# Kernel optimization log

Hardware: AMD Instinct MI355X
Metric: run time of the kernel (lower is better)

The kernel has to match this reference:

```python
import jax, jax.numpy as jnp
import numpy as np

S = 192          # spatial_size
N = 100000       # active input sites
CIN, M, M2, NCLS = 3, 32, 64, 50
EPS = 1e-4       # scn BatchNorm eps
OFFS = np.array([[dx, dy, dz] for dx in (-1, 0, 1) for dy in (-1, 0, 1) for dz in (-1, 0, 1)], dtype=np.int64)


def _build_nbr(coords, size):
    # coords: [n,3] unique int64. Returns [n,27] int32 neighbor index (-1 = inactive site),
    # i.e. the submanifold-convolution rulebook built via sorted-key hashing.
    n = coords.shape[0]
    keys = (coords[:, 0] * size + coords[:, 1]) * size + coords[:, 2]
    order = np.argsort(keys)
    sk = keys[order]
    nbr = np.full((n, 27), -1, dtype=np.int32)
    for k, off in enumerate(OFFS):
        nc = coords + off
        ok = np.all((nc >= 0) & (nc < size), axis=1)
        qk = (nc[:, 0] * size + nc[:, 1]) * size + nc[:, 2]
        pos = np.searchsorted(sk, qk).clip(0, n - 1)
        hit = ok & (sk[pos] == qk)
        nbr[hit, k] = order[pos[hit]].astype(np.int32)
    return nbr


def setup_inputs() -> dict:
    rng = np.random.default_rng(0)
    raw = rng.integers(0, S, size=(130000, 3), dtype=np.int64)
    keys = (raw[:, 0] * S + raw[:, 1]) * S + raw[:, 2]
    _, first = np.unique(keys, return_index=True)
    coords = raw[np.sort(first)][:N]          # N unique active voxels
    nbr_fine = _build_nbr(coords, S)
    # stride-2 / filter-2 downsample rulebook: coarse sites = unique(coords // 2)
    S2 = S // 2
    cc = coords // 2
    ckeys = (cc[:, 0] * S2 + cc[:, 1]) * S2 + cc[:, 2]
    uk, parent = np.unique(ckeys, return_inverse=True)
    ccoords = np.column_stack((uk // (S2 * S2), (uk // S2) % S2, uk % S2))
    nbr_coarse = _build_nbr(ccoords, S2)
    offset_id = (coords[:, 0] % 2) * 4 + (coords[:, 1] % 2) * 2 + coords[:, 2] % 2
    key = jax.random.key(0)
    ks = jax.random.split(key, 8)
    def w(k, shape, fan):
        return jax.random.normal(k, shape, jnp.float32) * (1.0 / np.sqrt(fan))
    return dict(
        coords=jnp.asarray(coords, jnp.int32),
        features=jax.random.normal(ks[0], (N, CIN), jnp.float32),
        nbr_fine=jnp.asarray(nbr_fine),
        nbr_coarse=jnp.asarray(nbr_coarse),
        parent=jnp.asarray(parent.astype(np.int32)),
        offset_id=jnp.asarray(offset_id.astype(np.int32)),
        num_coarse=int(uk.shape[0]),
        w_in=w(ks[1], (27, CIN, M), 27 * CIN),
        w_b1=w(ks[2], (27, M, M), 27 * M),
        w_down=w(ks[3], (8, M, M2), 8 * M),
        w_b2=w(ks[4], (27, M2, M2), 27 * M2),
        w_up=w(ks[5], (8, M2, M), 8 * M2),
        w_b3=w(ks[6], (27, 2 * M, M), 27 * 2 * M),
        g1=jnp.ones((M,)), b1=jnp.zeros((M,)),
        gd=jnp.ones((M,)), bd=jnp.zeros((M,)),
        g2=jnp.ones((M2,)), b2=jnp.zeros((M2,)),
        gu=jnp.ones((M2,)), bu=jnp.zeros((M2,)),
        g3=jnp.ones((2 * M,)), b3=jnp.zeros((2 * M,)),
        go=jnp.ones((M,)), bo=jnp.zeros((M,)),
        w_lin=w(ks[7], (M, NCLS), M),
        b_lin=jnp.zeros((NCLS,)),
    )


def _subm_conv(f, nbr, W):
    # f: [n,Cin], nbr: [n,27] (-1 = inactive), W: [27,Cin,Cout]
    mask = nbr >= 0
    g = f[jnp.where(mask, nbr, 0)] * mask[..., None]  # [n,27,Cin]
    return jnp.einsum('nkc,kcd->nd', g, W)


def _bnrelu(f, gamma, beta):
    mu = f.mean(0)
    var = ((f - mu) ** 2).mean(0)
    return jax.nn.relu((f - mu) * (gamma / jnp.sqrt(var + EPS)) + beta)


def _down(f, parent, off_id, W, nc):
    # strided 2^3 conv: out[parent] += W[offset(child)] @ f[child]
    out = jnp.zeros((nc, W.shape[2]), f.dtype)
    for o in range(8):
        sel = (off_id == o)[:, None].astype(f.dtype)
        out = out + jax.ops.segment_sum((f * sel) @ W[o], parent, num_segments=nc)
    return out


def _up(g, parent, off_id, W):
    # 2^3 deconv back to fine sites
    gp = g[parent]
    out = jnp.zeros((gp.shape[0], W.shape[2]), g.dtype)
    for o in range(8):
        out = out + (off_id == o)[:, None].astype(g.dtype) * (gp @ W[o])
    return out


def reference(coords, features, nbr_fine, nbr_coarse, parent, offset_id, num_coarse,
              w_in, w_b1, w_down, w_b2, w_up, w_b3,
              g1, b1, gd, bd, g2, b2, gu, bu, g3, b3, go, bo, w_lin, b_lin):
    # InputLayer (coords unique -> identity) + SubmanifoldConvolution(CIN->M)
    f = _subm_conv(features, nbr_fine, w_in)
    # UNet level 0 block (pre-activation)
    f = _subm_conv(_bnrelu(f, g1, b1), nbr_fine, w_b1)
    skip = f
    # downsample: BNReLU + Convolution(M->M2, 2, 2)
    g = _down(_bnrelu(f, gd, bd), parent, offset_id, w_down, num_coarse)
    # UNet level 1 block
    g = _subm_conv(_bnrelu(g, g2, b2), nbr_coarse, w_b2)
    # upsample: BNReLU + Deconvolution(M2->M, 2, 2)
    u = _up(_bnrelu(g, gu, bu), parent, offset_id, w_up)
    # JoinTable + block (2M -> M)
    f = jnp.concatenate([skip, u], axis=1)
    f = _subm_conv(_bnrelu(f, g3, b3), nbr_fine, w_b3)
    # top-level BatchNormReLU(M) + OutputLayer + Linear head
    f = _bnrelu(f, go, bo)
    return f @ w_lin + b_lin
```

## Files before the change

### kernel.cpp

```cpp
#include <hip/hip_runtime.h>

#define EPS_BN 1e-4f
constexpr int BLK = 256;
constexpr int ECAPC = 1856;
constexpr int NCOPY = 8;

__global__ __launch_bounds__(64) void build_fine_k(
    const int* __restrict__ nbr, int n, int* __restrict__ cnt, int* __restrict__ ent) {
  int i = blockIdx.x * 64 + threadIdx.x;
  if (i >= n) return;
  int c = 0;
  const int* nr = nbr + (size_t)i * 27;
  int* er = ent + (size_t)i * 27;
#pragma unroll 1
  for (int k = 0; k < 27; ++k) {
    int j = nr[k];
    if (j >= 0) er[c++] = (k << 18) | j;
  }
  cnt[i] = c;
}

__global__ __launch_bounds__(64) void build_subm4_k(
    const int* __restrict__ nbr, int n,
    int* __restrict__ segP, int* __restrict__ ent) {
  int T = blockIdx.x, r = threadIdx.x;
  int i = T * 64 + r;
  bool valid = i < n;
  int base = 0;
#pragma unroll 1
  for (int k = 0; k < 27; ++k) {
    int j = valid ? nbr[(size_t)i * 27 + k] : -1;
    bool act = j >= 0;
    unsigned long long mb = __ballot(act);
    int cntk = __popcll(mb);
    int pre = __popcll(mb & ((1ull << r) - 1));
    if (act) ent[(size_t)T * ECAPC + base + pre] = (r << 23) | (k << 18) | j;
    int padded = (cntk + 3) & ~3;
    if (r < padded - cntk) ent[(size_t)T * ECAPC + base + cntk + r] = -1;
    base += padded;
  }
  if (r == 0) segP[T] = base;
}

__global__ __launch_bounds__(BLK) void child_scatter_k(
    const int* __restrict__ parent, const int* __restrict__ offid, int n,
    int* __restrict__ ccnt, int* __restrict__ cent) {
  int i = blockIdx.x * BLK + threadIdx.x;
  if (i >= n) return;
  int p = parent[i];
  int slot = atomicAdd(&ccnt[p], 1);
  cent[p * 8 + slot] = i | (offid[i] << 25);
}

template <int CI, int CO, int MODE>
__global__ __launch_bounds__(BLK) void tconvA_k(
    const float* __restrict__ in, const int* __restrict__ ent, const int* __restrict__ cnt,
    const int* __restrict__ parent, const int* __restrict__ offid,
    const float* __restrict__ W, float* __restrict__ out, int n,
    float* __restrict__ osums) {
  constexpr int LANES = CO / 4, SLOTS = BLK / LANES, RPS = 64 / SLOTS;
  __shared__ float red[2 * CO];
  int t = threadIdx.x;
  for (int idx = t; idx < 2 * CO; idx += BLK) red[idx] = 0.f;
  __syncthreads();
  int slot = t / LANES, lane = t % LANES, g = lane * 4;
  int T = blockIdx.x;
  float ssum[4] = {0, 0, 0, 0}, ssq[4] = {0, 0, 0, 0};
#pragma unroll 1
  for (int rr = 0; rr < RPS; ++rr) {
    int row = T * 64 + slot * RPS + rr;
    bool vrow = row < n;
    float a0 = 0.f, a1 = 0.f, a2 = 0.f, a3 = 0.f;
    int ec = 0;
    if (vrow) ec = (MODE == 2) ? 1 : cnt[row];
#pragma unroll 1
    for (int e = 0; e < ec; ++e) {
      int k, j;
      if constexpr (MODE == 0) {
        int v = ent[(size_t)row * 27 + e];
        k = (v >> 18) & 31; j = v & 0x3FFFF;
      } else if constexpr (MODE == 1) {
        int v = ent[(size_t)row * 8 + e];
        k = v >> 25; j = v & 0x1FFFFFF;
      } else {
        k = offid[row]; j = parent[row];
      }
      const float* Wk = W + (size_t)k * (CI * CO) + g;
      const float* xr = in + (size_t)j * CI;
#pragma unroll
      for (int h = 0; h < CI / 32; ++h) {
        float4 xv[8];
#pragma unroll
        for (int c4 = 0; c4 < 8; ++c4)
          xv[c4] = *reinterpret_cast<const float4*>(xr + h * 32 + c4 * 4);
#pragma unroll
        for (int c4 = 0; c4 < 8; ++c4) {
          float xs[4] = {xv[c4].x, xv[c4].y, xv[c4].z, xv[c4].w};
#pragma unroll
          for (int q = 0; q < 4; ++q) {
            float4 wv = *reinterpret_cast<const float4*>(Wk + (size_t)(h * 32 + c4 * 4 + q) * CO);
            a0 = fmaf(xs[q], wv.x, a0);
            a1 = fmaf(xs[q], wv.y, a1);
            a2 = fmaf(xs[q], wv.z, a2);
            a3 = fmaf(xs[q], wv.w, a3);
          }
        }
      }
    }
    if (vrow)
      *reinterpret_cast<float4*>(out + (size_t)row * CO + g) = make_float4(a0, a1, a2, a3);
    ssum[0] += a0; ssum[1] += a1; ssum[2] += a2; ssum[3] += a3;
    ssq[0] = fmaf(a0, a0, ssq[0]); ssq[1] = fmaf(a1, a1, ssq[1]);
    ssq[2] = fmaf(a2, a2, ssq[2]); ssq[3] = fmaf(a3, a3, ssq[3]);
  }
#pragma unroll
  for (int q = 0; q < 4; ++q) {
    atomicAdd(&red[g + q], ssum[q]);
    atomicAdd(&red[CO + g + q], ssq[q]);
  }
  __syncthreads();
  int copy = blockIdx.x & (NCOPY - 1);
  if (t < 2 * CO) atomicAdd(&osums[copy * 2 * CO + t], red[t]);
}

template <int CI, int CO>
__global__ __launch_bounds__(BLK) void tconvB_k(
    const float* __restrict__ in, const int* __restrict__ segP,
    const int* __restrict__ ent, int ecap,
    const float* __restrict__ sums, const float* __restrict__ gm,
    const float* __restrict__ bt, float invn,
    const float* __restrict__ W, float* __restrict__ out, int n,
    float* __restrict__ osums) {
  constexpr int AP = CO + 2;
  constexpr int XP = CI + 2;
  constexpr int CHUNK = 128;
  __shared__ float lacc[64 * AP];
  __shared__ float lx[CHUNK * XP];
  __shared__ int   lent[CHUNK];
  __shared__ float lst[2 * CI];
  int t = threadIdx.x, T = blockIdx.x;
  if (t < CI) {
    float s = 0.f, q = 0.f;
#pragma unroll
    for (int cp = 0; cp < NCOPY; ++cp) { s += sums[cp * 2 * CI + t]; q += sums[cp * 2 * CI + CI + t]; }
    float mu = s * invn, var = q * invn - mu * mu;
    float sc = gm[t] / sqrtf(var + EPS_BN);
    lst[t] = sc; lst[CI + t] = bt[t] - mu * sc;
  }
  for (int idx = t; idx < 64 * AP; idx += BLK) lacc[idx] = 0.f;
  int P = segP[T];
  const int* entT = ent + (size_t)T * ecap;
  int slot = t >> 4, g = (t & 15) * 4;
  __syncthreads();

#pragma unroll 1
  for (int c0 = 0; c0 < P; c0 += CHUNK) {
    int lim = min(P - c0, CHUNK);
    if (t < CHUNK) lent[t] = (t < lim) ? entT[c0 + t] : -1;
    for (int idx = t; idx < CHUNK * 16; idx += BLK) {
      int pr = idx >> 4, cq = idx & 15;
      int ev = (pr < lim) ? entT[c0 + pr] : -1;
      float4 v = make_float4(0.f, 0.f, 0.f, 0.f);
      if (ev >= 0) {
        int j = ev & 0x3FFFF;
        float4 x = *reinterpret_cast<const float4*>(in + (size_t)j * CI + cq * 4);
        int cb = cq * 4;
        float y0 = fmaf(x.x, lst[cb + 0], lst[CI + cb + 0]);
        float y1 = fmaf(x.y, lst[cb + 1], lst[CI + cb + 1]);
        float y2 = fmaf(x.z, lst[cb + 2], lst[CI + cb + 2]);
        float y3 = fmaf(x.w, lst[cb + 3], lst[CI + cb + 3]);
        v = make_float4(y0 > 0.f ? y0 : 0.f, y1 > 0.f ? y1 : 0.f,
                        y2 > 0.f ? y2 : 0.f, y3 > 0.f ? y3 : 0.f);
      }
      *reinterpret_cast<float4*>(&lx[pr * XP + cq * 4]) = v;
    }
    __syncthreads();
#pragma unroll 1
    for (int gr = slot; gr * 4 < lim; gr += 16) {
      int p0 = gr * 4;
      int e0 = lent[p0];
      int k = (e0 >> 18) & 31;
      const float* Wk = W + (size_t)k * (CI * CO) + g;
      int rr[4];
      float acc[4][4];
#pragma unroll
      for (int pp = 0; pp < 4; ++pp) {
        int ev = lent[p0 + pp];
        rr[pp] = ev >= 0 ? ((ev >> 23) & 63) : -1;
        acc[pp][0] = acc[pp][1] = acc[pp][2] = acc[pp][3] = 0.f;
      }
#pragma unroll 4
      for (int c4 = 0; c4 < CI / 4; ++c4) {
        int cb = c4 * 4;
        float xs[4][4];
#pragma unroll
        for (int pp = 0; pp < 4; ++pp) {
          float4 xv = *reinterpret_cast<const float4*>(&lx[(p0 + pp) * XP + cb]);
          xs[pp][0] = xv.x; xs[pp][1] = xv.y; xs[pp][2] = xv.z; xs[pp][3] = xv.w;
        }
#pragma unroll
        for (int q = 0; q < 4; ++q) {
          float4 w4 = *reinterpret_cast<const float4*>(Wk + (size_t)(cb + q) * CO);
#pragma unroll
          for (int pp = 0; pp < 4; ++pp) {
            acc[pp][0] = fmaf(xs[pp][q], w4.x, acc[pp][0]);
            acc[pp][1] = fmaf(xs[pp][q], w4.y, acc[pp][1]);
            acc[pp][2] = fmaf(xs[pp][q], w4.z, acc[pp][2]);
            acc[pp][3] = fmaf(xs[pp][q], w4.w, acc[pp][3]);
          }
        }
      }
#pragma unroll
      for (int pp = 0; pp < 4; ++pp) {
        if (rr[pp] >= 0) {
          float* ap = &lacc[rr[pp] * AP + g];
          atomicAdd(ap + 0, acc[pp][0]);
          atomicAdd(ap + 1, acc[pp][1]);
          atomicAdd(ap + 2, acc[pp][2]);
          atomicAdd(ap + 3, acc[pp][3]);
        }
      }
    }
    __syncthreads();
  }

  for (int idx = t; idx < 64 * (CO / 4); idx += BLK) {
    int r = idx / (CO / 4), c4 = idx - r * (CO / 4);
    int row = T * 64 + r;
    if (row < n)
      *reinterpret_cast<float4*>(out + (size_t)row * CO + c4 * 4) =
          *reinterpret_cast<const float4*>(&lacc[r * AP + c4 * 4]);
  }
  int copy = blockIdx.x & (NCOPY - 1);
  if (t < CO) {
    float s = 0.f, ss = 0.f;
#pragma unroll 4
    for (int r = 0; r < 64; ++r) {
      float x = lacc[r * AP + t];
      s += x; ss = fmaf(x, x, ss);
    }
    atomicAdd(&osums[copy * 2 * CO + t], s);
    atomicAdd(&osums[copy * 2 * CO + CO + t], ss);
  }
}

template <int C>
__global__ __launch_bounds__(BLK) void bnact_k(
    const float* __restrict__ in, const float* __restrict__ sums,
    const float* __restrict__ gm, const float* __restrict__ bt, float invn,
    float* __restrict__ outp, int n) {
  __shared__ float lst[2 * C];
  int t = threadIdx.x;
  if (t < C) {
    float s = 0.f, q = 0.f;
#pragma unroll
    for (int cp = 0; cp < NCOPY; ++cp) { s += sums[cp * 2 * C + t]; q += sums[cp * 2 * C + C + t]; }
    float mu = s * invn, var = q * invn - mu * mu;
    float sc = gm[t] / sqrtf(var + EPS_BN);
    lst[t] = sc; lst[C + t] = bt[t] - mu * sc;
  }
  __syncthreads();
  int total = n * (C / 4);
  const float4* in4 = reinterpret_cast<const float4*>(in);
  float4* out4 = reinterpret_cast<float4*>(outp);
  for (int idx = blockIdx.x * BLK + t; idx < total; idx += gridDim.x * BLK) {
    int cb = (idx & (C / 4 - 1)) * 4;
    float4 x = in4[idx];
    float v[4] = {x.x, x.y, x.z, x.w};
#pragma unroll
    for (int q = 0; q < 4; ++q) {
      float y = fmaf(v[q], lst[cb + q], lst[C + cb + q]);
      v[q] = y > 0.f ? y : 0.f;
    }
    out4[idx] = make_float4(v[0], v[1], v[2], v[3]);
  }
}

__global__ __launch_bounds__(BLK) void bncat_k(
    const float* __restrict__ fa, const float* __restrict__ sA,
    const float* __restrict__ gA, const float* __restrict__ bA,
    const float* __restrict__ fb, const float* __restrict__ sB,
    const float* __restrict__ gB, const float* __restrict__ bB,
    float invn, float* __restrict__ acat, int n) {
  __shared__ float lst[128];
  int t = threadIdx.x;
  if (t < 64) {
    int half = t >> 5, c = t & 31;
    const float* ss = half ? sB : sA;
    const float* gg = half ? gB : gA;
    const float* bb = half ? bB : bA;
    float s = 0.f, q = 0.f;
#pragma unroll
    for (int cp = 0; cp < NCOPY; ++cp) { s += ss[cp * 64 + c]; q += ss[cp * 64 + 32 + c]; }
    float mu = s * invn, var = q * invn - mu * mu;
    float sc = gg[c] / sqrtf(var + EPS_BN);
    lst[half * 64 + c] = sc; lst[half * 64 + 32 + c] = bb[c] - mu * sc;
  }
  __syncthreads();
  int total = n * 16;
  for (int idx = blockIdx.x * BLK + t; idx < total; idx += gridDim.x * BLK) {
    int row = idx >> 4, c4 = idx & 15;
    int half = c4 >> 3, cc = (c4 & 7) * 4;
    const float* src = half ? fb : fa;
    float4 x = *reinterpret_cast<const float4*>(src + (size_t)row * 32 + cc);
    const float* L = lst + half * 64;
    float v[4] = {x.x, x.y, x.z, x.w};
#pragma unroll
    for (int q = 0; q < 4; ++q) {
      float y = fmaf(v[q], L[cc + q], L[32 + cc + q]);
      v[q] = y > 0.f ? y : 0.f;
    }
    *reinterpret_cast<float4*>(acat + (size_t)row * 64 + c4 * 4) = make_float4(v[0], v[1], v[2], v[3]);
  }
}

__global__ __launch_bounds__(BLK) void conv_in_k(
    const float* __restrict__ feat, const int* __restrict__ nbr,
    const float* __restrict__ W, float* __restrict__ out, int n,
    float* __restrict__ osums) {
  int i = blockIdx.x * BLK + threadIdx.x;
  bool valid = i < n;
  float acc[32];
#pragma unroll
  for (int c = 0; c < 32; ++c) acc[c] = 0.f;
#pragma unroll 1
  for (int k = 0; k < 27; ++k) {
    int j = valid ? nbr[(size_t)i * 27 + k] : -1;
    if (j < 0) continue;
    float x0 = feat[j * 3 + 0], x1 = feat[j * 3 + 1], x2 = feat[j * 3 + 2];
    const float* w0 = W + k * 96;
#pragma unroll
    for (int co = 0; co < 8; ++co) {
      float4 a = *reinterpret_cast<const float4*>(w0 + co * 4);
      float4 b = *reinterpret_cast<const float4*>(w0 + 32 + co * 4);
      float4 cc = *reinterpret_cast<const float4*>(w0 + 64 + co * 4);
      acc[4*co+0] = fmaf(x0, a.x, fmaf(x1, b.x, fmaf(x2, cc.x, acc[4*co+0])));
      acc[4*co+1] = fmaf(x0, a.y, fmaf(x1, b.y, fmaf(x2, cc.y, acc[4*co+1])));
      acc[4*co+2] = fmaf(x0, a.z, fmaf(x1, b.z, fmaf(x2, cc.z, acc[4*co+2])));
      acc[4*co+3] = fmaf(x0, a.w, fmaf(x1, b.w, fmaf(x2, cc.w, acc[4*co+3])));
    }
  }
  if (valid) {
    float* o = out + (size_t)i * 32;
#pragma unroll
    for (int co = 0; co < 8; ++co)
      *reinterpret_cast<float4*>(o + co * 4) = make_float4(acc[4*co], acc[4*co+1], acc[4*co+2], acc[4*co+3]);
  }
  __shared__ float red[2][4][32];
  int w = threadIdx.x >> 6;
#pragma unroll
  for (int c = 0; c < 32; ++c) {
    float v = acc[c], q = acc[c] * acc[c];
#pragma unroll
    for (int off = 32; off; off >>= 1) {
      v += __shfl_down(v, off);
      q += __shfl_down(q, off);
    }
    if ((threadIdx.x & 63) == 0) { red[0][w][c] = v; red[1][w][c] = q; }
  }
  __syncthreads();
  if (threadIdx.x < 64) {
    int kind = threadIdx.x >> 5, c = threadIdx.x & 31;
    float s = red[kind][0][c] + red[kind][1][c] + red[kind][2][c] + red[kind][3][c];
    atomicAdd(&osums[(blockIdx.x & (NCOPY - 1)) * 64 + kind * 32 + c], s);
  }
}

__global__ __launch_bounds__(BLK) void head_k(
    const float* __restrict__ fin, const float* __restrict__ sums,
    const float* __restrict__ gm, const float* __restrict__ bt, float inv_n,
    const float* __restrict__ Wl, const float* __restrict__ bl,
    float* __restrict__ out, int n) {
  __shared__ float lw[32 * 50];
  __shared__ float lb[52];
  __shared__ float lst[64];
  int t = threadIdx.x;
  if (t < 32) {
    float s = 0.f, q = 0.f;
#pragma unroll
    for (int cp = 0; cp < NCOPY; ++cp) { s += sums[cp * 64 + t]; q += sums[cp * 64 + 32 + t]; }
    float mu = s * inv_n, var = q * inv_n - mu * mu;
    float sc = gm[t] / sqrtf(var + EPS_BN);
    lst[t] = sc; lst[32 + t] = bt[t] - mu * sc;
  }
  for (int idx = t; idx < 1600; idx += BLK) lw[idx] = Wl[idx];
  if (t < 50) lb[t] = bl[t];
  __syncthreads();
  int i = blockIdx.x * BLK + t;
  if (i >= n) return;
  float x[32];
  const float* fj = fin + (size_t)i * 32;
#pragma unroll
  for (int c4 = 0; c4 < 8; ++c4) {
    float4 v = *reinterpret_cast<const float4*>(fj + c4 * 4);
    float vs[4] = {v.x, v.y, v.z, v.w};
#pragma unroll
    for (int q = 0; q < 4; ++q) {
      int c = c4 * 4 + q;
      float y = fmaf(vs[q], lst[c], lst[32 + c]);
      x[c] = y > 0.f ? y : 0.f;
    }
  }
  float acc[50];
#pragma unroll
  for (int co = 0; co < 50; ++co) acc[co] = lb[co];
#pragma unroll 4
  for (int c = 0; c < 32; ++c) {
#pragma unroll
    for (int co = 0; co < 50; ++co) acc[co] = fmaf(x[c], lw[c * 50 + co], acc[co]);
  }
  float* o = out + (size_t)i * 50;
#pragma unroll
  for (int co = 0; co < 25; ++co)
    *reinterpret_cast<float2*>(o + co * 2) = make_float2(acc[co * 2], acc[co * 2 + 1]);
}

extern "C" void kernel_launch(void* const* d_in, const int* in_sizes, int n_in,
                              void* d_out, int out_size, void* d_ws, size_t ws_size,
                              hipStream_t stream) {
  const float* feat   = (const float*)d_in[1];
  const int*   nbrF   = (const int*)d_in[2];
  const int*   nbrC   = (const int*)d_in[3];
  const int*   parent = (const int*)d_in[4];
  const int*   offid  = (const int*)d_in[5];
  const float* w_in   = (const float*)d_in[7];
  const float* w_b1   = (const float*)d_in[8];
  const float* w_down = (const float*)d_in[9];
  const float* w_b2   = (const float*)d_in[10];
  const float* w_up   = (const float*)d_in[11];
  const float* w_b3   = (const float*)d_in[12];
  const float* g1v = (const float*)d_in[13], *b1v = (const float*)d_in[14];
  const float* gdv = (const float*)d_in[15], *bdv = (const float*)d_in[16];
  const float* g2v = (const float*)d_in[17], *b2v = (const float*)d_in[18];
  const float* guv = (const float*)d_in[19], *buv = (const float*)d_in[20];
  const float* g3v = (const float*)d_in[21], *b3v = (const float*)d_in[22];
  const float* gov = (const float*)d_in[23], *bov = (const float*)d_in[24];
  const float* w_lin = (const float*)d_in[25];
  const float* b_lin = (const float*)d_in[26];
  float* out = (float*)d_out;

  int N  = in_sizes[4];
  int NC = in_sizes[3] / 27;
  int ntF = (N + 63) / 64, ntC = (NC + 63) / 64;

  size_t szF = (size_t)N * 32;
  size_t szG = (size_t)NC * 64;
  size_t SB  = (size_t)N * 64;

  float* ws = (float*)d_ws;
  float* S1 = ws;
  float* S2 = S1 + SB;
  float* S3 = S2 + SB;
  float* S4 = S3 + szF;
  float* S5 = S4 + szF;
  float* sums1 = S5 + szG;
  float* sumsD = sums1 + 8 * 64;
  float* sums2 = sumsD + 8 * 64;
  float* sumsU = sums2 + 8 * 128;
  float* sums4 = sumsU + 8 * 128;
  float* sums5 = sums4 + 8 * 64;
  int* ccnt = (int*)(sums5 + 8 * 64);
  int* cent = ccnt + NC;
  int* cntF = cent + (size_t)NC * 8;
  int* entF = cntF + N;
  int* segPC = entF + (size_t)N * 27;
  int* entC  = segPC + ntC;

  hipMemsetAsync(sums1, 0, (4096 + NC) * sizeof(float), stream);

  int gridN = (N + BLK - 1) / BLK;
  int agrid = 1024;
  float invN = 1.f / (float)N, invC = 1.f / (float)NC;

  build_fine_k<<<ntF, 64, 0, stream>>>(nbrF, N, cntF, entF);
  build_subm4_k<<<ntC, 64, 0, stream>>>(nbrC, NC, segPC, entC);
  child_scatter_k<<<gridN, BLK, 0, stream>>>(parent, offid, N, ccnt, cent);

  conv_in_k<<<gridN, BLK, 0, stream>>>(feat, nbrF, w_in, S1, N, sums1);
  bnact_k<32><<<agrid, BLK, 0, stream>>>(S1, sums1, g1v, b1v, invN, S2, N);

  tconvA_k<32, 32, 0><<<ntF, BLK, 0, stream>>>(
      S2, entF, cntF, nullptr, nullptr, w_b1, S3, N, sumsD);
  bnact_k<32><<<agrid, BLK, 0, stream>>>(S3, sumsD, gdv, bdv, invN, S4, N);

  tconvA_k<32, 64, 1><<<ntC, BLK, 0, stream>>>(
      S4, cent, ccnt, nullptr, nullptr, w_down, S5, NC, sums2);

  tconvB_k<64, 64><<<ntC, BLK, 0, stream>>>(
      S5, segPC, entC, ECAPC, sums2, g2v, b2v, invC, w_b2, S1, NC, sumsU);
  bnact_k<64><<<agrid, BLK, 0, stream>>>(S1, sumsU, guv, buv, invC, S5, NC);

  tconvA_k<64, 32, 2><<<ntF, BLK, 0, stream>>>(
      S5, nullptr, nullptr, parent, offid, w_up, S4, N, sums4);

  bncat_k<<<agrid, BLK, 0, stream>>>(
      S3, sumsD, g3v, b3v, S4, sums4, g3v + 32, b3v + 32, invN, S2, N);

  tconvA_k<64, 32, 0><<<ntF, BLK, 0, stream>>>(
      S2, entF, cntF, nullptr, nullptr, w_b3, S3, N, sums5);

  head_k<<<gridN, BLK, 0, stream>>>(S3, sums5, gov, bov, invN, w_lin, b_lin, out, N);
}
```

Before: 552.8 us.

## Restructure coarse subm conv: per-offset segments, LDS-staged weights, 128-row tiles

Measured after the change: 581.0 us. +5.1%, slower.

```diff
diff --git a/kernel.cpp b/kernel.cpp
--- a/kernel.cpp
+++ b/kernel.cpp
@@ -2,7 +2,7 @@
 
 #define EPS_BN 1e-4f
 constexpr int BLK = 256;
-constexpr int ECAPC = 1856;
+constexpr int ECAPC = 1728;
 constexpr int NCOPY = 8;
 
 __global__ __launch_bounds__(64) void build_fine_k(
@@ -20,26 +20,24 @@
   cnt[i] = c;
 }
 
-__global__ __launch_bounds__(64) void build_subm4_k(
+__global__ __launch_bounds__(64) void build_subm_k(
     const int* __restrict__ nbr, int n,
-    int* __restrict__ segP, int* __restrict__ ent) {
+    int* __restrict__ seg, int* __restrict__ ent) {
   int T = blockIdx.x, r = threadIdx.x;
   int i = T * 64 + r;
   bool valid = i < n;
   int base = 0;
+  if (r == 0) seg[T * 28] = 0;
 #pragma unroll 1
   for (int k = 0; k < 27; ++k) {
     int j = valid ? nbr[(size_t)i * 27 + k] : -1;
     bool act = j >= 0;
     unsigned long long mb = __ballot(act);
-    int cntk = __popcll(mb);
     int pre = __popcll(mb & ((1ull << r) - 1));
-    if (act) ent[(size_t)T * ECAPC + base + pre] = (r << 23) | (k << 18) | j;
-    int padded = (cntk + 3) & ~3;
-    if (r < padded - cntk) ent[(size_t)T * ECAPC + base + cntk + r] = -1;
-    base += padded;
-  }
-  if (r == 0) segP[T] = base;
+    if (act) ent[(size_t)T * ECAPC + base + pre] = (r << 22) | j;
+    base += __popcll(mb);
+    if (r == 0) seg[T * 28 + k + 1] = base;
+  }
 }
 
 __global__ __launch_bounds__(BLK) void child_scatter_k(
@@ -125,20 +123,23 @@
 
 template <int CI, int CO>
 __global__ __launch_bounds__(BLK) void tconvB_k(
-    const float* __restrict__ in, const int* __restrict__ segP,
-    const int* __restrict__ ent, int ecap,
+    const float* __restrict__ in, const int* __restrict__ seg,
+    const int* __restrict__ ent, int ecap, int ntiles,
     const float* __restrict__ sums, const float* __restrict__ gm,
     const float* __restrict__ bt, float invn,
     const float* __restrict__ W, float* __restrict__ out, int n,
     float* __restrict__ osums) {
-  constexpr int AP = CO + 2;
-  constexpr int XP = CI + 2;
-  constexpr int CHUNK = 128;
-  __shared__ float lacc[64 * AP];
-  __shared__ float lx[CHUNK * XP];
-  __shared__ int   lent[CHUNK];
+  constexpr int AP = CO + 4;
+  constexpr int XP = CI + 4;
+  constexpr int CAP = 64;
+  constexpr int WL = CI * CO / 4 / BLK;
+  __shared__ float lacc[128 * AP];
+  __shared__ float lw[CI * CO];
+  __shared__ float lx[CAP * XP];
+  __shared__ int   lr[CAP];
   __shared__ float lst[2 * CI];
   int t = threadIdx.x, T = blockIdx.x;
+
   if (t < CI) {
     float s = 0.f, q = 0.f;
 #pragma unroll
@@ -147,86 +148,110 @@
     float sc = gm[t] / sqrtf(var + EPS_BN);
     lst[t] = sc; lst[CI + t] = bt[t] - mu * sc;
   }
-  for (int idx = t; idx < 64 * AP; idx += BLK) lacc[idx] = 0.f;
-  int P = segP[T];
-  const int* entT = ent + (size_t)T * ecap;
-  int slot = t >> 4, g = (t & 15) * 4;
-  __syncthreads();
-
-#pragma unroll 1
-  for (int c0 = 0; c0 < P; c0 += CHUNK) {
-    int lim = min(P - c0, CHUNK);
-    if (t < CHUNK) lent[t] = (t < lim) ? entT[c0 + t] : -1;
-    for (int idx = t; idx < CHUNK * 16; idx += BLK) {
-      int pr = idx >> 4, cq = idx & 15;
-      int ev = (pr < lim) ? entT[c0 + pr] : -1;
-      float4 v = make_float4(0.f, 0.f, 0.f, 0.f);
-      if (ev >= 0) {
-        int j = ev & 0x3FFFF;
+  for (int idx = t; idx < 128 * AP; idx += BLK) lacc[idx] = 0.f;
+
+  int TA = 2 * T, TB = 2 * T + 1;
+  bool hasB = TB < ntiles;
+  const int* segA = seg + TA * 28;
+  const int* segB = seg + (hasB ? TB : TA) * 28;
+  const int* entA = ent + (size_t)TA * ecap;
+  const int* entB = ent + (size_t)(hasB ? TB : TA) * ecap;
+
+  int k = 27, a0 = 0, a1 = 0, b0 = 0, b1 = 0;
+#pragma unroll 1
+  for (int kk = 0; kk < 27; ++kk) {
+    int x0 = segA[kk], x1 = segA[kk + 1];
+    int y0 = hasB ? segB[kk] : 0, y1 = hasB ? segB[kk + 1] : 0;
+    if (x1 > x0 || y1 > y0) { k = kk; a0 = x0; a1 = x1; b0 = y0; b1 = y1; break; }
+  }
+  float4 wreg[WL];
+  if (k < 27) {
+    const float4* wsrc = reinterpret_cast<const float4*>(W + (size_t)k * CI * CO);
+#pragma unroll
+    for (int q = 0; q < WL; ++q) wreg[q] = wsrc[t + q * BLK];
+  }
+  __syncthreads();
+
+#pragma unroll 1
+  while (k < 27) {
+#pragma unroll
+    for (int q = 0; q < WL; ++q)
+      reinterpret_cast<float4*>(lw)[t + q * BLK] = wreg[q];
+    int kn = 27, c0 = 0, c1 = 0, d0 = 0, d1 = 0;
+#pragma unroll 1
+    for (int kk = k + 1; kk < 27; ++kk) {
+      int x0 = segA[kk], x1 = segA[kk + 1];
+      int y0 = hasB ? segB[kk] : 0, y1 = hasB ? segB[kk + 1] : 0;
+      if (x1 > x0 || y1 > y0) { kn = kk; c0 = x0; c1 = x1; d0 = y0; d1 = y1; break; }
+    }
+    if (kn < 27) {
+      const float4* wsrc = reinterpret_cast<const float4*>(W + (size_t)kn * CI * CO);
+#pragma unroll
+      for (int q = 0; q < WL; ++q) wreg[q] = wsrc[t + q * BLK];
+    }
+    int mA = a1 - a0, m = mA + (b1 - b0);
+    int done = 0;
+#pragma unroll 1
+    while (done < m) {
+      int mc = min(m - done, CAP);
+      if (t < CAP) {
+        int r = -1;
+        if (t < mc) {
+          int p = done + t;
+          int e = (p < mA) ? entA[a0 + p] : entB[b0 + p - mA];
+          r = (e >> 22) + ((p < mA) ? 0 : 64);
+        }
+        lr[t] = r;
+      }
+      for (int idx = t; idx < mc * 16; idx += BLK) {
+        int pr = idx >> 4, cq = idx & 15;
+        int p = done + pr;
+        int e = (p < mA) ? entA[a0 + p] : entB[b0 + p - mA];
+        int j = e & 0x3FFFFF;
         float4 x = *reinterpret_cast<const float4*>(in + (size_t)j * CI + cq * 4);
         int cb = cq * 4;
         float y0 = fmaf(x.x, lst[cb + 0], lst[CI + cb + 0]);
         float y1 = fmaf(x.y, lst[cb + 1], lst[CI + cb + 1]);
         float y2 = fmaf(x.z, lst[cb + 2], lst[CI + cb + 2]);
         float y3 = fmaf(x.w, lst[cb + 3], lst[CI + cb + 3]);
-        v = make_float4(y0 > 0.f ? y0 : 0.f, y1 > 0.f ? y1 : 0.f,
+        *reinterpret_cast<float4*>(&lx[pr * XP + cb]) =
+            make_float4(y0 > 0.f ? y0 : 0.f, y1 > 0.f ? y1 : 0.f,
                         y2 > 0.f ? y2 : 0.f, y3 > 0.f ? y3 : 0.f);
       }
-      *reinterpret_cast<float4*>(&lx[pr * XP + cq * 4]) = v;
-    }
-    __syncthreads();
-#pragma unroll 1
-    for (int gr = slot; gr * 4 < lim; gr += 16) {
-      int p0 = gr * 4;
-      int e0 = lent[p0];
-      int k = (e0 >> 18) & 31;
-      const float* Wk = W + (size_t)k * (CI * CO) + g;
-      int rr[4];
-      float acc[4][4];
-#pragma unroll
-      for (int pp = 0; pp < 4; ++pp) {
-        int ev = lent[p0 + pp];
-        rr[pp] = ev >= 0 ? ((ev >> 23) & 63) : -1;
-        acc[pp][0] = acc[pp][1] = acc[pp][2] = acc[pp][3] = 0.f;
-      }
+      __syncthreads();
+      int slot = t >> 4, g = (t & 15) * 4;
+#pragma unroll 1
+      for (int p = slot; p < mc; p += 16) {
+        int r = lr[p];
+        float acc0 = 0.f, acc1 = 0.f, acc2 = 0.f, acc3 = 0.f;
 #pragma unroll 4
-      for (int c4 = 0; c4 < CI / 4; ++c4) {
-        int cb = c4 * 4;
-        float xs[4][4];
-#pragma unroll
-        for (int pp = 0; pp < 4; ++pp) {
-          float4 xv = *reinterpret_cast<const float4*>(&lx[(p0 + pp) * XP + cb]);
-          xs[pp][0] = xv.x; xs[pp][1] = xv.y; xs[pp][2] = xv.z; xs[pp][3] = xv.w;
-        }
-#pragma unroll
-        for (int q = 0; q < 4; ++q) {
-          float4 w4 = *reinterpret_cast<const float4*>(Wk + (size_t)(cb + q) * CO);
-#pragma unroll
-          for (int pp = 0; pp < 4; ++pp) {
-            acc[pp][0] = fmaf(xs[pp][q], w4.x, acc[pp][0]);
-            acc[pp][1] = fmaf(xs[pp][q], w4.y, acc[pp][1]);
-            acc[pp][2] = fmaf(xs[pp][q], w4.z, acc[pp][2]);
-            acc[pp][3] = fmaf(xs[pp][q], w4.w, acc[pp][3]);
+        for (int c4 = 0; c4 < CI / 4; ++c4) {
+          int cb = c4 * 4;
+          float4 xv = *reinterpret_cast<const float4*>(&lx[p * XP + cb]);
+          float xs[4] = {xv.x, xv.y, xv.z, xv.w};
+#pragma unroll
+          for (int q = 0; q < 4; ++q) {
+            float4 wv = *reinterpret_cast<const float4*>(&lw[(cb + q) * CO + g]);
+            acc0 = fmaf(xs[q], wv.x, acc0);
+            acc1 = fmaf(xs[q], wv.y, acc1);
+            acc2 = fmaf(xs[q], wv.z, acc2);
+            acc3 = fmaf(xs[q], wv.w, acc3);
           }
         }
+        float* ap = &lacc[r * AP + g];
+        float4 old = *reinterpret_cast<float4*>(ap);
+        *reinterpret_cast<float4*>(ap) =
+            make_float4(old.x + acc0, old.y + acc1, old.z + acc2, old.w + acc3);
       }
-#pragma unroll
-      for (int pp = 0; pp < 4; ++pp) {
-        if (rr[pp] >= 0) {
-          float* ap = &lacc[rr[pp] * AP + g];
-          atomicAdd(ap + 0, acc[pp][0]);
-          atomicAdd(ap + 1, acc[pp][1]);
-          atomicAdd(ap + 2, acc[pp][2]);
-          atomicAdd(ap + 3, acc[pp][3]);
-        }
-      }
-    }
-    __syncthreads();
-  }
-
-  for (int idx = t; idx < 64 * (CO / 4); idx += BLK) {
+      __syncthreads();
+      done += mc;
+    }
+    k = kn; a0 = c0; a1 = c1; b0 = d0; b1 = d1;
+  }
+
+  for (int idx = t; idx < 128 * (CO / 4); idx += BLK) {
     int r = idx / (CO / 4), c4 = idx - r * (CO / 4);
-    int row = T * 64 + r;
+    int row = T * 128 + r;
     if (row < n)
       *reinterpret_cast<float4*>(out + (size_t)row * CO + c4 * 4) =
           *reinterpret_cast<const float4*>(&lacc[r * AP + c4 * 4]);
@@ -235,7 +260,7 @@
   if (t < CO) {
     float s = 0.f, ss = 0.f;
 #pragma unroll 4
-    for (int r = 0; r < 64; ++r) {
+    for (int r = 0; r < 128; ++r) {
       float x = lacc[r * AP + t];
       s += x; ss = fmaf(x, x, ss);
     }
@@ -442,6 +467,7 @@
   int N  = in_sizes[4];
   int NC = in_sizes[3] / 27;
   int ntF = (N + 63) / 64, ntC = (NC + 63) / 64;
+  int ntC2 = (NC + 127) / 128;
 
   size_t szF = (size_t)N * 32;
   size_t szG = (size_t)NC * 64;
@@ -464,7 +490,7 @@
   int* cntF = cent + (size_t)NC * 8;
   int* entF = cntF + N;
   int* segPC = entF + (size_t)N * 27;
-  int* entC  = segPC + ntC;
+  int* entC  = segPC + (size_t)ntC * 28;
 
   hipMemsetAsync(sums1, 0, (4096 + NC) * sizeof(float), stream);
 
@@ -473,7 +499,7 @@
   float invN = 1.f / (float)N, invC = 1.f / (float)NC;
 
   build_fine_k<<<ntF, 64, 0, stream>>>(nbrF, N, cntF, entF);
-  build_subm4_k<<<ntC, 64, 0, stream>>>(nbrC, NC, segPC, entC);
+  build_subm_k<<<ntC, 64, 0, stream>>>(nbrC, NC, segPC, entC);
   child_scatter_k<<<gridN, BLK, 0, stream>>>(parent, offid, N, ccnt, cent);
 
   conv_in_k<<<gridN, BLK, 0, stream>>>(feat, nbrF, w_in, S1, N, sums1);
@@ -486,8 +512,8 @@
   tconvA_k<32, 64, 1><<<ntC, BLK, 0, stream>>>(
       S4, cent, ccnt, nullptr, nullptr, w_down, S5, NC, sums2);
 
-  tconvB_k<64, 64><<<ntC, BLK, 0, stream>>>(
-      S5, segPC, entC, ECAPC, sums2, g2v, b2v, invC, w_b2, S1, NC, sumsU);
+  tconvB_k<64, 64><<<ntC2, BLK, 0, stream>>>(
+      S5, segPC, entC, ECAPC, ntC, sums2, g2v, b2v, invC, w_b2, S1, NC, sumsU);
   bnact_k<64><<<agrid, BLK, 0, stream>>>(S1, sumsU, guv, buv, invC, S5, NC);
 
   tconvA_k<64, 32, 2><<<ntF, BLK, 0, stream>>>(
```
